# Performance work log

Measured on AMD Instinct MI355X. Metric: run time of the kernel, lower is better.

## Reference

```python
import jax, jax.numpy as jnp
import numpy as np

N, E, D, H, O = 50000, 800000, 128, 128, 64


def setup_inputs() -> dict:
    key = jax.random.key(0)
    ks = jax.random.split(key, 16)
    x = jax.random.normal(ks[0], (N, D), jnp.float32)
    edge_index = jax.random.randint(ks[1], (2, E), 0, N, dtype=jnp.int32).astype(jnp.int64)

    def lin_w(k, out_d, in_d):
        return jax.random.normal(k, (out_d, in_d), jnp.float32) * (1.0 / np.sqrt(in_d))

    return {
        "x": x,
        "edge_index": edge_index,
        # SAGEConv layer 0 (D -> H): lin_l acts on aggregated neighbors (with bias), lin_r on root (no bias)
        "Wl0": lin_w(ks[2], H, D), "bl0": jnp.zeros((H,), jnp.float32), "Wr0": lin_w(ks[3], H, D),
        # SAGEConv layers 1,2 (H -> H)
        "Wl1": lin_w(ks[4], H, H), "bl1": jnp.zeros((H,), jnp.float32), "Wr1": lin_w(ks[5], H, H),
        "Wl2": lin_w(ks[6], H, H), "bl2": jnp.zeros((H,), jnp.float32), "Wr2": lin_w(ks[7], H, H),
        # post_mp: Linear(H,H) -> Dropout -> Linear(H,O)
        "Wp1": lin_w(ks[8], H, H), "bp1": jnp.zeros((H,), jnp.float32),
        "Wp2": lin_w(ks[9], O, H), "bp2": jnp.zeros((O,), jnp.float32),
    }


def _sage_conv(x, src, dst, W_l, b_l, W_r, n_nodes):
    # mean-aggregate neighbor features: scatter messages x[src] onto dst
    msgs = x[src]                                              # [E, F] gather
    agg = jax.ops.segment_sum(msgs, dst, num_segments=n_nodes)  # [N, F]
    cnt = jax.ops.segment_sum(jnp.ones((src.shape[0],), x.dtype), dst, num_segments=n_nodes)
    mean = agg / jnp.maximum(cnt, 1.0)[:, None]
    return mean @ W_l.T + b_l + x @ W_r.T


def reference(x, edge_index, Wl0, bl0, Wr0, Wl1, bl1, Wr1, Wl2, bl2, Wr2, Wp1, bp1, Wp2, bp2):
    src, dst = edge_index[0], edge_index[1]
    n_nodes = x.shape[0]
    layers = [(Wl0, bl0, Wr0), (Wl1, bl1, Wr1), (Wl2, bl2, Wr2)]
    h = x
    for (W_l, b_l, W_r) in layers:
        h = _sage_conv(h, src, dst, W_l, b_l, W_r, n_nodes)
        h = jax.nn.relu(h)
        # dropout is identity at inference (training=False)
    h = h @ Wp1.T + bp1
    h = h @ Wp2.T + bp2
    return jax.nn.log_softmax(h, axis=1)
```

## Files before the change

kernel.cpp:

```cpp
#include <hip/hip_runtime.h>

using s16x8 = __attribute__((ext_vector_type(8))) short;
using f32x4 = __attribute__((ext_vector_type(4))) float;

#define NBUKMAX 512
#define BCAP    3072
#define CHUNK   4096

static __device__ __forceinline__ float bf2f(unsigned short u){
  union { unsigned int i; float f; } v; v.i = ((unsigned)u) << 16; return v.f;
}
static __device__ __forceinline__ unsigned short f2bf(float f){
  union { float f; unsigned int i; } v; v.f = f;
  unsigned int x = v.i;
  return (unsigned short)((x + 0x7fffu + ((x >> 16) & 1u)) >> 16);
}

__global__ __launch_bounds__(256) void k_bscatter(const int* __restrict__ ei, int E,
                                                  int* __restrict__ gcur,
                                                  unsigned int* __restrict__ tmp){
  __shared__ unsigned int pk[CHUNK];
  __shared__ unsigned short bk[CHUNK];
  __shared__ int hist[NBUKMAX];
  __shared__ int cur[NBUKMAX];
  __shared__ int sh64;
  int tid = threadIdx.x;
  if (tid == 0) sh64 = 1;
  for (int j = tid; j < NBUKMAX; j += 256) hist[j] = 0;
  __syncthreads();
  {
    int nc = E < 64 ? E : 64;
    if (tid < nc && ei[2*tid + 1] != 0) sh64 = 0;
  }
  __syncthreads();
  int is64 = sh64;
  int base = blockIdx.x * CHUNK;
  int m = E - base; if (m > CHUNK) m = CHUNK;
  for (int j = tid; j < m; j += 256){
    int i = base + j;
    int s = is64 ? ei[2*(size_t)i] : ei[i];
    int d = is64 ? ei[2*((size_t)E + i)] : ei[(size_t)E + i];
    pk[j] = ((unsigned)(d & 127) << 25) | (unsigned)s;
    int b = d >> 7;
    bk[j] = (unsigned short)b;
    atomicAdd(&hist[b], 1);
  }
  __syncthreads();
  for (int b = tid; b < NBUKMAX; b += 256){
    int r = hist[b];
    cur[b] = (r > 0) ? atomicAdd(&gcur[b], r) : 0;
  }
  __syncthreads();
  for (int j = tid; j < m; j += 256){
    int b = bk[j];
    int p = atomicAdd(&cur[b], 1);
    if (p < BCAP) tmp[(size_t)b*BCAP + p] = pk[j];
  }
}

__global__ __launch_bounds__(256) void k_binfill(const unsigned int* __restrict__ tmp,
                                                 const int* __restrict__ gcur,
                                                 int* __restrict__ rowp,
                                                 int* __restrict__ srcs, int N, int nbk){
  __shared__ int hist[128], cur[128];
  __shared__ unsigned int stg[BCAP];
  __shared__ int lout[BCAP];
  __shared__ int sh_obase;
  int b = blockIdx.x;
  int d0 = b << 7;
  int nd = N - d0; if (nd > 128) nd = 128;
  int n = gcur[b]; if (n > BCAP) n = BCAP; if (n < 0) n = 0;
  int tid = threadIdx.x;
  for (int j = tid; j < 128; j += 256) hist[j] = 0;
  if (tid < 64){
    int lane = tid;
    int carry = 0;
    for (int b0 = 0; b0 <= b; b0 += 64){
      int bb = b0 + lane;
      int sz = 0;
      if (bb < nbk){ sz = gcur[bb]; if (sz > BCAP) sz = BCAP; if (sz < 0) sz = 0; }
      int s = sz;
      #pragma unroll
      for (int off = 1; off < 64; off <<= 1){
        int u = __shfl_up(s, off, 64);
        if (lane >= off) s += u;
      }
      if (bb == b) sh_obase = carry + s - sz;
      carry += __shfl(s, 63, 64);
    }
  }
  __syncthreads();
  int obase = sh_obase;
  const unsigned int* reg = tmp + (size_t)b * BCAP;
  for (int i = tid; i < n; i += 256){
    unsigned int w = reg[i];
    stg[i] = w;
    atomicAdd(&hist[w >> 25], 1);
  }
  __syncthreads();
  if (tid < 64){
    int a  = hist[2*tid];
    int b2 = hist[2*tid+1];
    int ps = a + b2;
    int s = ps;
    #pragma unroll
    for (int off = 1; off < 64; off <<= 1){
      int u = __shfl_up(s, off, 64);
      if (tid >= off) s += u;
    }
    int ep = s - ps;
    cur[2*tid]   = ep;
    cur[2*tid+1] = ep + a;
    if (2*tid   < nd) rowp[d0 + 2*tid]   = obase + ep;
    if (2*tid+1 < nd) rowp[d0 + 2*tid+1] = obase + ep + a;
  }
  if (b == nbk - 1 && tid == 0) rowp[N] = obase + n;
  __syncthreads();
  for (int i = tid; i < n; i += 256){
    unsigned int w = stg[i];
    int p = atomicAdd(&cur[w >> 25], 1);
    lout[p] = (int)(w & 0x1FFFFFFu);
  }
  __syncthreads();
  for (int i = tid; i < n; i += 256) srcs[obase + i] = lout[i];
}

__global__ __launch_bounds__(256) void k_prep(const float* __restrict__ x, unsigned short* __restrict__ xb, int n4, int nx,
                                              const float* __restrict__ w0, const float* __restrict__ w1,
                                              const float* __restrict__ w2, const float* __restrict__ w3,
                                              const float* __restrict__ w4, const float* __restrict__ w5,
                                              unsigned short* __restrict__ o0, unsigned short* __restrict__ o1,
                                              unsigned short* __restrict__ o2, unsigned short* __restrict__ o3,
                                              unsigned short* __restrict__ o4, unsigned short* __restrict__ o5,
                                              const float* __restrict__ Wp1, const float* __restrict__ bp1,
                                              const float* __restrict__ Wp2, const float* __restrict__ bp2,
                                              unsigned short* __restrict__ Wc, float* __restrict__ bc){
  int bx = blockIdx.x;
  if (bx < nx){
    int i = bx*256 + threadIdx.x;
    if (i >= n4) return;
    float4 v = ((const float4*)x)[i];
    ushort4 o; o.x = f2bf(v.x); o.y = f2bf(v.y); o.z = f2bf(v.z); o.w = f2bf(v.w);
    ((ushort4*)xb)[i] = o;
  } else if (bx < nx + 96){
    int w = bx - nx;
    int job = w >> 4, blk = w & 15;
    const float* in; unsigned short* out;
    switch (job){
      case 0: in = w0; out = o0; break;
      case 1: in = w1; out = o1; break;
      case 2: in = w2; out = o2; break;
      case 3: in = w3; out = o3; break;
      case 4: in = w4; out = o4; break;
      default: in = w5; out = o5; break;
    }
    int i = blk*256 + threadIdx.x;
    float4 v = ((const float4*)in)[i];
    ushort4 o; o.x = f2bf(v.x); o.y = f2bf(v.y); o.z = f2bf(v.z); o.w = f2bf(v.w);
    ((ushort4*)out)[i] = o;
  } else {
    int idx = (bx - nx - 96)*256 + threadIdx.x;
    if (idx >= 64*128) return;
    int o = idx >> 7, k = idx & 127;
    float s = 0.f;
    for (int j = 0; j < 128; ++j) s += Wp2[o*128 + j] * Wp1[j*128 + k];
    Wc[o*128 + k] = f2bf(s);
    if (k == 0){
      float t = bp2[o];
      for (int j = 0; j < 128; ++j) t += Wp2[o*128 + j] * bp1[j];
      bc[o] = t;
    }
  }
}

__global__ __launch_bounds__(256) void k_agg(const unsigned short* __restrict__ h,
                                             const int* __restrict__ rowp,
                                             const int* __restrict__ srcs,
                                             unsigned short* __restrict__ mean, int N){
  int wv = blockIdx.x*4 + (threadIdx.x >> 6);
  int n0 = wv*2;
  if (n0 >= N) return;
  int n1 = n0 + 1;
  int lane = threadIdx.x & 63;
  int g  = lane >> 4;
  int fl = lane & 15;
  int beg0 = rowp[n0], end0 = rowp[n0+1];
  int beg1 = beg0, end1 = beg0;
  if (n1 < N){ beg1 = rowp[n1]; end1 = rowp[n1+1]; }
  int deg0 = end0 - beg0, deg1 = end1 - beg1;
  int it0 = (deg0 + 15) >> 4, it1 = (deg1 + 15) >> 4;
  int it = it0 > it1 ? it0 : it1;
  int c0 = deg0 > 0 ? end0 - 1 : 0;
  int c1 = deg1 > 0 ? end1 - 1 : 0;
  float a0[8], a1[8];
  #pragma unroll
  for (int f = 0; f < 8; ++f){ a0[f] = 0.f; a1[f] = 0.f; }
  for (int t = 0; t < it; ++t){
    int b0 = beg0 + t*16, b1 = beg1 + t*16;
    int si0[4], si1[4]; float w0[4], w1[4];
    #pragma unroll
    for (int s = 0; s < 4; ++s){
      int sl0 = b0 + s*4 + g;
      w0[s] = (sl0 < end0) ? 1.f : 0.f;
      si0[s] = srcs[sl0 < end0 ? sl0 : c0];
      int sl1 = b1 + s*4 + g;
      w1[s] = (sl1 < end1) ? 1.f : 0.f;
      si1[s] = srcs[sl1 < end1 ? sl1 : c1];
    }
    uint4 v0[4], v1[4];
    #pragma unroll
    for (int s = 0; s < 4; ++s) v0[s] = *(const uint4*)(h + (size_t)si0[s]*128 + fl*8);
    #pragma unroll
    for (int s = 0; s < 4; ++s) v1[s] = *(const uint4*)(h + (size_t)si1[s]*128 + fl*8);
    #pragma unroll
    for (int s = 0; s < 4; ++s){
      #pragma unroll
      for (int q = 0; q < 4; ++q){
        unsigned int wd = ((const unsigned int*)&v0[s])[q];
        a0[2*q]   = fmaf(w0[s], bf2f((unsigned short)(wd & 0xffffu)), a0[2*q]);
        a0[2*q+1] = fmaf(w0[s], bf2f((unsigned short)(wd >> 16)),     a0[2*q+1]);
        wd = ((const unsigned int*)&v1[s])[q];
        a1[2*q]   = fmaf(w1[s], bf2f((unsigned short)(wd & 0xffffu)), a1[2*q]);
        a1[2*q+1] = fmaf(w1[s], bf2f((unsigned short)(wd >> 16)),     a1[2*q+1]);
      }
    }
  }
  #pragma unroll
  for (int f = 0; f < 8; ++f){
    a0[f] += __shfl_xor(a0[f], 16, 64);
    a0[f] += __shfl_xor(a0[f], 32, 64);
    a1[f] += __shfl_xor(a1[f], 16, 64);
    a1[f] += __shfl_xor(a1[f], 32, 64);
  }
  if (g == 0){
    float inv0 = deg0 > 0 ? 1.f/(float)deg0 : 0.f;
    unsigned int o[4];
    #pragma unroll
    for (int q = 0; q < 4; ++q)
      o[q] = ((unsigned int)f2bf(a0[2*q+1]*inv0) << 16) | f2bf(a0[2*q]*inv0);
    *(uint4*)(mean + (size_t)n0*128 + fl*8) = *(uint4*)&o[0];
    if (n1 < N){
      float inv1 = deg1 > 0 ? 1.f/(float)deg1 : 0.f;
      #pragma unroll
      for (int q = 0; q < 4; ++q)
        o[q] = ((unsigned int)f2bf(a1[2*q+1]*inv1) << 16) | f2bf(a1[2*q]*inv1);
      *(uint4*)(mean + (size_t)n1*128 + fl*8) = *(uint4*)&o[0];
    }
  }
}

__global__ __launch_bounds__(256) void k_gemm(const unsigned short* __restrict__ mean,
                                              const unsigned short* __restrict__ hin,
                                              const unsigned short* __restrict__ Wl,
                                              const unsigned short* __restrict__ Wr,
                                              const float* __restrict__ bias,
                                              unsigned short* __restrict__ hout, int N){
  __shared__ unsigned short wlds[64*512];
  int wave = threadIdx.x >> 6;
  int lane = threadIdx.x & 63;
  int lr = lane & 15;
  int kg = lane >> 4;

  #pragma unroll
  for (int cc = 0; cc < 16; ++cc){
    int c = wave + cc*4;
    const unsigned short* W = (c < 32) ? Wl : Wr;
    int jt = (c >> 2) & 7, t = c & 3;
    s16x8 v = *(const s16x8*)(W + (size_t)(jt*16 + lr)*128 + t*32 + kg*8);
    *(s16x8*)(wlds + (size_t)c*512 + lane*8) = v;
  }
  __syncthreads();

  int row0 = (blockIdx.x*4 + wave) * 16;
  if (row0 >= N) return;
  int row = row0 + lr; if (row >= N) row = N - 1;

  s16x8 a[8];
  const unsigned short* mrow = mean + (size_t)row*128;
  const unsigned short* hrow = hin  + (size_t)row*128;
  #pragma unroll
  for (int t = 0; t < 4; ++t) a[t]   = *(const s16x8*)(mrow + t*32 + kg*8);
  #pragma unroll
  for (int t = 0; t < 4; ++t) a[4+t] = *(const s16x8*)(hrow + t*32 + kg*8);

  #pragma unroll
  for (int jt = 0; jt < 8; ++jt){
    f32x4 acc = {0.f, 0.f, 0.f, 0.f};
    #pragma unroll
    for (int t = 0; t < 4; ++t){
      s16x8 b = *(const s16x8*)(wlds + (size_t)(jt*4 + t)*512 + lane*8);
      acc = __builtin_amdgcn_mfma_f32_16x16x32_bf16(a[t], b, acc, 0, 0, 0);
    }
    #pragma unroll
    for (int t = 0; t < 4; ++t){
      s16x8 b = *(const s16x8*)(wlds + (size_t)(32 + jt*4 + t)*512 + lane*8);
      acc = __builtin_amdgcn_mfma_f32_16x16x32_bf16(a[4+t], b, acc, 0, 0, 0);
    }
    int ocol = jt*16 + lr;
    float bv = bias[ocol];
    #pragma unroll
    for (int i = 0; i < 4; ++i){
      int orow = row0 + kg*4 + i;
      if (orow < N){
        float v = acc[i] + bv;
        v = fmaxf(v, 0.f);
        hout[(size_t)orow*128 + ocol] = f2bf(v);
      }
    }
  }
}

__global__ __launch_bounds__(256) void k_gemmpost(const unsigned short* __restrict__ mean,
                                                  const unsigned short* __restrict__ hin,
                                                  const unsigned short* __restrict__ Wl,
                                                  const unsigned short* __restrict__ Wr,
                                                  const float* __restrict__ bias,
                                                  const unsigned short* __restrict__ Wc,
                                                  const float* __restrict__ bc,
                                                  float* __restrict__ out, int N){
  __shared__ unsigned short wlds[64*512];
  int wave = threadIdx.x >> 6;
  int lane = threadIdx.x & 63;
  int lr = lane & 15;
  int kg = lane >> 4;

  #pragma unroll
  for (int cc = 0; cc < 16; ++cc){
    int c = wave + cc*4;
    const unsigned short* W = (c < 32) ? Wl : Wr;
    int jt = (c >> 2) & 7, t = c & 3;
    s16x8 v = *(const s16x8*)(W + (size_t)(jt*16 + lr)*128 + t*32 + kg*8);
    *(s16x8*)(wlds + (size_t)c*512 + lane*8) = v;
  }
  __syncthreads();

  int row0 = (blockIdx.x*4 + wave) * 16;
  int row = row0 + lr; if (row >= N) row = N - 1;

  s16x8 a[8];
  const unsigned short* mrow = mean + (size_t)row*128;
  const unsigned short* hrow = hin  + (size_t)row*128;
  #pragma unroll
  for (int t = 0; t < 4; ++t) a[t]   = *(const s16x8*)(mrow + t*32 + kg*8);
  #pragma unroll
  for (int t = 0; t < 4; ++t) a[4+t] = *(const s16x8*)(hrow + t*32 + kg*8);

  f32x4 acc2[8];
  #pragma unroll
  for (int jt = 0; jt < 8; ++jt){
    f32x4 acc = {0.f, 0.f, 0.f, 0.f};
    #pragma unroll
    for (int t = 0; t < 4; ++t){
      s16x8 b = *(const s16x8*)(wlds + (size_t)(jt*4 + t)*512 + lane*8);
      acc = __builtin_amdgcn_mfma_f32_16x16x32_bf16(a[t], b, acc, 0, 0, 0);
    }
    #pragma unroll
    for (int t = 0; t < 4; ++t){
      s16x8 b = *(const s16x8*)(wlds + (size_t)(32 + jt*4 + t)*512 + lane*8);
      acc = __builtin_amdgcn_mfma_f32_16x16x32_bf16(a[4+t], b, acc, 0, 0, 0);
    }
    acc2[jt] = acc;
  }
  __syncthreads();

  unsigned short* tl = wlds + (size_t)wave * (16*136);
  #pragma unroll
  for (int jt = 0; jt < 8; ++jt){
    float bv = bias[jt*16 + lr];
    #pragma unroll
    for (int i = 0; i < 4; ++i){
      float v = fmaxf(acc2[jt][i] + bv, 0.f);
      tl[(kg*4 + i)*136 + jt*16 + lr] = f2bf(v);
    }
  }
  s16x8 am[4];
  #pragma unroll
  for (int t = 0; t < 4; ++t)
    am[t] = *(const s16x8*)(tl + lr*136 + t*32 + kg*8);

  float vv[4][4];
  #pragma unroll
  for (int jt = 0; jt < 4; ++jt){
    f32x4 acc = {0.f, 0.f, 0.f, 0.f};
    const unsigned short* wrow = Wc + (size_t)(jt*16 + lr)*128;
    #pragma unroll
    for (int t = 0; t < 4; ++t){
      s16x8 b = *(const s16x8*)(wrow + t*32 + kg*8);
      acc = __builtin_amdgcn_mfma_f32_16x16x32_bf16(am[t], b, acc, 0, 0, 0);
    }
    float bv = bc[jt*16 + lr];
    #pragma unroll
    for (int i = 0; i < 4; ++i) vv[jt][i] = acc[i] + bv;
  }

  #pragma unroll
  for (int i = 0; i < 4; ++i){
    float m = vv[0][i];
    #pragma unroll
    for (int jt = 1; jt < 4; ++jt) m = fmaxf(m, vv[jt][i]);
    #pragma unroll
    for (int msk = 1; msk < 16; msk <<= 1) m = fmaxf(m, __shfl_xor(m, msk, 64));
    float s = 0.f;
    #pragma unroll
    for (int jt = 0; jt < 4; ++jt) s += expf(vv[jt][i] - m);
    #pragma unroll
    for (int msk = 1; msk < 16; msk <<= 1) s += __shfl_xor(s, msk, 64);
    float lse = m + logf(s);
    int orow = row0 + kg*4 + i;
    if (orow < N){
      #pragma unroll
      for (int jt = 0; jt < 4; ++jt)
        out[(size_t)orow*64 + jt*16 + lr] = vv[jt][i] - lse;
    }
  }
}

extern "C" void kernel_launch(void* const* d_in, const int* in_sizes, int n_in,
                              void* d_out, int out_size, void* d_ws, size_t ws_size,
                              hipStream_t stream){
  const int N = in_sizes[0] / 128;
  const int E = in_sizes[1] / 2;
  if (N <= 0 || E <= 0) return;

  const float* x   = (const float*)d_in[0];
  const int*   ei  = (const int*)d_in[1];
  const float* Wl[3] = {(const float*)d_in[2], (const float*)d_in[5], (const float*)d_in[8]};
  const float* bl[3] = {(const float*)d_in[3], (const float*)d_in[6], (const float*)d_in[9]};
  const float* Wr[3] = {(const float*)d_in[4], (const float*)d_in[7], (const float*)d_in[10]};
  const float* Wp1 = (const float*)d_in[11];
  const float* bp1 = (const float*)d_in[12];
  const float* Wp2 = (const float*)d_in[13];
  const float* bp2 = (const float*)d_in[14];
  float* out = (float*)d_out;

  char* p = (char*)d_ws;
  auto alloc = [&](size_t bytes){ char* r = p; p += (bytes + 255) & ~(size_t)255; return r; };
  unsigned short* xb   = (unsigned short*)alloc((size_t)N*128*2);
  unsigned short* hA   = (unsigned short*)alloc((size_t)N*128*2);
  unsigned short* hB   = (unsigned short*)alloc((size_t)N*128*2);
  unsigned short* mean = (unsigned short*)alloc((size_t)N*128*2);
  unsigned short* wlb[3], *wrb[3];
  for (int l = 0; l < 3; ++l){
    wlb[l] = (unsigned short*)alloc(128*128*2);
    wrb[l] = (unsigned short*)alloc(128*128*2);
  }
  unsigned short* wc = (unsigned short*)alloc(64*128*2);
  float* bc   = (float*)alloc(64*4);
  int* rowp   = (int*)alloc((size_t)(N+1)*4);
  int* srcs   = (int*)alloc((size_t)E*4);
  int* gcur   = (int*)alloc((size_t)NBUKMAX*4);
  unsigned int* tmp = (unsigned int*)alloc((size_t)NBUKMAX*BCAP*4);

  int nbk = (N + 127) >> 7;

  hipMemsetAsync(gcur, 0, (size_t)NBUKMAX*4, stream);
  k_bscatter<<<(E + CHUNK - 1)/CHUNK, 256, 0, stream>>>(ei, E, gcur, tmp);
  k_binfill<<<nbk, 256, 0, stream>>>(tmp, gcur, rowp, srcs, N, nbk);

  int n4 = N*128/4;
  int nx = (n4 + 255)/256;
  k_prep<<<nx + 96 + 32, 256, 0, stream>>>(x, xb, n4, nx,
                                           Wl[0], Wr[0], Wl[1], Wr[1], Wl[2], Wr[2],
                                           wlb[0], wrb[0], wlb[1], wrb[1], wlb[2], wrb[2],
                                           Wp1, bp1, Wp2, bp2, wc, bc);

  int waves = (N + 15)/16;
  int gblocks = (waves + 3)/4;
  int ablocks = (N + 7)/8;
  k_agg<<<ablocks, 256, 0, stream>>>(xb, rowp, srcs, mean, N);
  k_gemm<<<gblocks, 256, 0, stream>>>(mean, xb, wlb[0], wrb[0], bl[0], hA, N);
  k_agg<<<ablocks, 256, 0, stream>>>(hA, rowp, srcs, mean, N);
  k_gemm<<<gblocks, 256, 0, stream>>>(mean, hA, wlb[1], wrb[1], bl[1], hB, N);
  k_agg<<<ablocks, 256, 0, stream>>>(hB, rowp, srcs, mean, N);
  k_gemmpost<<<gblocks, 256, 0, stream>>>(mean, hB, wlb[2], wrb[2], bl[2], wc, bc, out, N);
}
```

Baseline: 212.3 us.

## Merge edge bucketing with prep kernel and aggregate one node per wave

The edge-bucket scatter kernel and the bf16 conversion/weight-prep kernel become one launch, so the independent front-end work shares a grid and one launch is dropped. The aggregation kernel now gives each wave a single node instead of two interleaved nodes, with an early exit for zero-degree nodes, and doubles the aggregation grid. This removes the wasted iterations spent padding the shorter of two neighbour lists. In exchange there is less memory-level parallelism per wave, and the fused front kernel reserves the scatter path's shared memory for every block.

```diff
diff --git a/kernel.cpp b/kernel.cpp
--- a/kernel.cpp
+++ b/kernel.cpp
@@ -16,45 +16,92 @@
   return (unsigned short)((x + 0x7fffu + ((x >> 16) & 1u)) >> 16);
 }
 
-__global__ __launch_bounds__(256) void k_bscatter(const int* __restrict__ ei, int E,
-                                                  int* __restrict__ gcur,
-                                                  unsigned int* __restrict__ tmp){
-  __shared__ unsigned int pk[CHUNK];
-  __shared__ unsigned short bk[CHUNK];
-  __shared__ int hist[NBUKMAX];
-  __shared__ int cur[NBUKMAX];
-  __shared__ int sh64;
+__global__ __launch_bounds__(256) void k_front(const int* __restrict__ ei, int E, int nbs,
+                                               int* __restrict__ gcur, unsigned int* __restrict__ tmp,
+                                               const float* __restrict__ x, unsigned short* __restrict__ xb,
+                                               int n4, int nx,
+                                               const float* __restrict__ w0, const float* __restrict__ w1,
+                                               const float* __restrict__ w2, const float* __restrict__ w3,
+                                               const float* __restrict__ w4, const float* __restrict__ w5,
+                                               unsigned short* __restrict__ o0, unsigned short* __restrict__ o1,
+                                               unsigned short* __restrict__ o2, unsigned short* __restrict__ o3,
+                                               unsigned short* __restrict__ o4, unsigned short* __restrict__ o5,
+                                               const float* __restrict__ Wp1, const float* __restrict__ bp1,
+                                               const float* __restrict__ Wp2, const float* __restrict__ bp2,
+                                               unsigned short* __restrict__ Wc, float* __restrict__ bc){
+  int bx = blockIdx.x;
   int tid = threadIdx.x;
-  if (tid == 0) sh64 = 1;
-  for (int j = tid; j < NBUKMAX; j += 256) hist[j] = 0;
-  __syncthreads();
-  {
-    int nc = E < 64 ? E : 64;
-    if (tid < nc && ei[2*tid + 1] != 0) sh64 = 0;
-  }
-  __syncthreads();
-  int is64 = sh64;
-  int base = blockIdx.x * CHUNK;
-  int m = E - base; if (m > CHUNK) m = CHUNK;
-  for (int j = tid; j < m; j += 256){
-    int i = base + j;
-    int s = is64 ? ei[2*(size_t)i] : ei[i];
-    int d = is64 ? ei[2*((size_t)E + i)] : ei[(size_t)E + i];
-    pk[j] = ((unsigned)(d & 127) << 25) | (unsigned)s;
-    int b = d >> 7;
-    bk[j] = (unsigned short)b;
-    atomicAdd(&hist[b], 1);
-  }
-  __syncthreads();
-  for (int b = tid; b < NBUKMAX; b += 256){
-    int r = hist[b];
-    cur[b] = (r > 0) ? atomicAdd(&gcur[b], r) : 0;
-  }
-  __syncthreads();
-  for (int j = tid; j < m; j += 256){
-    int b = bk[j];
-    int p = atomicAdd(&cur[b], 1);
-    if (p < BCAP) tmp[(size_t)b*BCAP + p] = pk[j];
+  if (bx < nbs){
+    __shared__ unsigned int pk[CHUNK];
+    __shared__ unsigned short bk[CHUNK];
+    __shared__ int hist[NBUKMAX];
+    __shared__ int cur[NBUKMAX];
+    __shared__ int sh64;
+    if (tid == 0) sh64 = 1;
+    for (int j = tid; j < NBUKMAX; j += 256) hist[j] = 0;
+    __syncthreads();
+    {
+      int nc = E < 64 ? E : 64;
+      if (tid < nc && ei[2*tid + 1] != 0) sh64 = 0;
+    }
+    __syncthreads();
+    int is64 = sh64;
+    int base = bx * CHUNK;
+    int m = E - base; if (m > CHUNK) m = CHUNK;
+    for (int j = tid; j < m; j += 256){
+      int i = base + j;
+      int s = is64 ? ei[2*(size_t)i] : ei[i];
+      int d = is64 ? ei[2*((size_t)E + i)] : ei[(size_t)E + i];
+      pk[j] = ((unsigned)(d & 127) << 25) | (unsigned)s;
+      int b = d >> 7;
+      bk[j] = (unsigned short)b;
+      atomicAdd(&hist[b], 1);
+    }
+    __syncthreads();
+    for (int b = tid; b < NBUKMAX; b += 256){
+      int r = hist[b];
+      cur[b] = (r > 0) ? atomicAdd(&gcur[b], r) : 0;
+    }
+    __syncthreads();
+    for (int j = tid; j < m; j += 256){
+      int b = bk[j];
+      int p = atomicAdd(&cur[b], 1);
+      if (p < BCAP) tmp[(size_t)b*BCAP + p] = pk[j];
+    }
+  } else if (bx < nbs + nx){
+    int i = (bx - nbs)*256 + tid;
+    if (i >= n4) return;
+    float4 v = ((const float4*)x)[i];
+    ushort4 o; o.x = f2bf(v.x); o.y = f2bf(v.y); o.z = f2bf(v.z); o.w = f2bf(v.w);
+    ((ushort4*)xb)[i] = o;
+  } else if (bx < nbs + nx + 96){
+    int w = bx - nbs - nx;
+    int job = w >> 4, blk = w & 15;
+    const float* in; unsigned short* out;
+    switch (job){
+      case 0: in = w0; out = o0; break;
+      case 1: in = w1; out = o1; break;
+      case 2: in = w2; out = o2; break;
+      case 3: in = w3; out = o3; break;
+      case 4: in = w4; out = o4; break;
+      default: in = w5; out = o5; break;
+    }
+    int i = blk*256 + tid;
+    float4 v = ((const float4*)in)[i];
+    ushort4 o; o.x = f2bf(v.x); o.y = f2bf(v.y); o.z = f2bf(v.z); o.w = f2bf(v.w);
+    ((ushort4*)out)[i] = o;
+  } else {
+    int idx = (bx - nbs - nx - 96)*256 + tid;
+    if (idx >= 64*128) return;
+    int o = idx >> 7, k = idx & 127;
+    float s = 0.f;
+    for (int j = 0; j < 128; ++j) s += Wp2[o*128 + j] * Wp1[j*128 + k];
+    Wc[o*128 + k] = f2bf(s);
+    if (k == 0){
+      float t = bp2[o];
+      for (int j = 0; j < 128; ++j) t += Wp2[o*128 + j] * bp1[j];
+      bc[o] = t;
+    }
   }
 }
 
@@ -125,127 +172,60 @@
   for (int i = tid; i < n; i += 256) srcs[obase + i] = lout[i];
 }
 
-__global__ __launch_bounds__(256) void k_prep(const float* __restrict__ x, unsigned short* __restrict__ xb, int n4, int nx,
-                                              const float* __restrict__ w0, const float* __restrict__ w1,
-                                              const float* __restrict__ w2, const float* __restrict__ w3,
-                                              const float* __restrict__ w4, const float* __restrict__ w5,
-                                              unsigned short* __restrict__ o0, unsigned short* __restrict__ o1,
-                                              unsigned short* __restrict__ o2, unsigned short* __restrict__ o3,
-                                              unsigned short* __restrict__ o4, unsigned short* __restrict__ o5,
-                                              const float* __restrict__ Wp1, const float* __restrict__ bp1,
-                                              const float* __restrict__ Wp2, const float* __restrict__ bp2,
-                                              unsigned short* __restrict__ Wc, float* __restrict__ bc){
-  int bx = blockIdx.x;
-  if (bx < nx){
-    int i = bx*256 + threadIdx.x;
-    if (i >= n4) return;
-    float4 v = ((const float4*)x)[i];
-    ushort4 o; o.x = f2bf(v.x); o.y = f2bf(v.y); o.z = f2bf(v.z); o.w = f2bf(v.w);
-    ((ushort4*)xb)[i] = o;
-  } else if (bx < nx + 96){
-    int w = bx - nx;
-    int job = w >> 4, blk = w & 15;
-    const float* in; unsigned short* out;
-    switch (job){
-      case 0: in = w0; out = o0; break;
-      case 1: in = w1; out = o1; break;
-      case 2: in = w2; out = o2; break;
-      case 3: in = w3; out = o3; break;
-      case 4: in = w4; out = o4; break;
-      default: in = w5; out = o5; break;
-    }
-    int i = blk*256 + threadIdx.x;
-    float4 v = ((const float4*)in)[i];
-    ushort4 o; o.x = f2bf(v.x); o.y = f2bf(v.y); o.z = f2bf(v.z); o.w = f2bf(v.w);
-    ((ushort4*)out)[i] = o;
-  } else {
-    int idx = (bx - nx - 96)*256 + threadIdx.x;
-    if (idx >= 64*128) return;
-    int o = idx >> 7, k = idx & 127;
-    float s = 0.f;
-    for (int j = 0; j < 128; ++j) s += Wp2[o*128 + j] * Wp1[j*128 + k];
-    Wc[o*128 + k] = f2bf(s);
-    if (k == 0){
-      float t = bp2[o];
-      for (int j = 0; j < 128; ++j) t += Wp2[o*128 + j] * bp1[j];
-      bc[o] = t;
-    }
-  }
-}
-
 __global__ __launch_bounds__(256) void k_agg(const unsigned short* __restrict__ h,
                                              const int* __restrict__ rowp,
                                              const int* __restrict__ srcs,
                                              unsigned short* __restrict__ mean, int N){
-  int wv = blockIdx.x*4 + (threadIdx.x >> 6);
-  int n0 = wv*2;
-  if (n0 >= N) return;
-  int n1 = n0 + 1;
+  int node = blockIdx.x*4 + (threadIdx.x >> 6);
+  if (node >= N) return;
   int lane = threadIdx.x & 63;
   int g  = lane >> 4;
   int fl = lane & 15;
-  int beg0 = rowp[n0], end0 = rowp[n0+1];
-  int beg1 = beg0, end1 = beg0;
-  if (n1 < N){ beg1 = rowp[n1]; end1 = rowp[n1+1]; }
-  int deg0 = end0 - beg0, deg1 = end1 - beg1;
-  int it0 = (deg0 + 15) >> 4, it1 = (deg1 + 15) >> 4;
-  int it = it0 > it1 ? it0 : it1;
-  int c0 = deg0 > 0 ? end0 - 1 : 0;
-  int c1 = deg1 > 0 ? end1 - 1 : 0;
-  float a0[8], a1[8];
-  #pragma unroll
-  for (int f = 0; f < 8; ++f){ a0[f] = 0.f; a1[f] = 0.f; }
-  for (int t = 0; t < it; ++t){
-    int b0 = beg0 + t*16, b1 = beg1 + t*16;
-    int si0[4], si1[4]; float w0[4], w1[4];
+  int beg = rowp[node], end = rowp[node+1];
+  int deg = end - beg;
+  if (deg <= 0){
+    if (g == 0){
+      uint4 z = make_uint4(0,0,0,0);
+      *(uint4*)(mean + (size_t)node*128 + fl*8) = z;
+    }
+    return;
+  }
+  float acc[8];
+  #pragma unroll
+  for (int f = 0; f < 8; ++f) acc[f] = 0.f;
+  int last = end - 1;
+  for (int base = beg; base < end; base += 16){
+    int si[4]; float w[4]; uint4 v[4];
     #pragma unroll
     for (int s = 0; s < 4; ++s){
-      int sl0 = b0 + s*4 + g;
-      w0[s] = (sl0 < end0) ? 1.f : 0.f;
-      si0[s] = srcs[sl0 < end0 ? sl0 : c0];
-      int sl1 = b1 + s*4 + g;
-      w1[s] = (sl1 < end1) ? 1.f : 0.f;
-      si1[s] = srcs[sl1 < end1 ? sl1 : c1];
-    }
-    uint4 v0[4], v1[4];
-    #pragma unroll
-    for (int s = 0; s < 4; ++s) v0[s] = *(const uint4*)(h + (size_t)si0[s]*128 + fl*8);
-    #pragma unroll
-    for (int s = 0; s < 4; ++s) v1[s] = *(const uint4*)(h + (size_t)si1[s]*128 + fl*8);
+      int sl = base + s*4 + g;
+      w[s] = (sl < end) ? 1.f : 0.f;
+      si[s] = srcs[sl < end ? sl : last];
+    }
+    #pragma unroll
+    for (int s = 0; s < 4; ++s) v[s] = *(const uint4*)(h + (size_t)si[s]*128 + fl*8);
     #pragma unroll
     for (int s = 0; s < 4; ++s){
       #pragma unroll
       for (int q = 0; q < 4; ++q){
-        unsigned int wd = ((const unsigned int*)&v0[s])[q];
-        a0[2*q]   = fmaf(w0[s], bf2f((unsigned short)(wd & 0xffffu)), a0[2*q]);
-        a0[2*q+1] = fmaf(w0[s], bf2f((unsigned short)(wd >> 16)),     a0[2*q+1]);
-        wd = ((const unsigned int*)&v1[s])[q];
-        a1[2*q]   = fmaf(w1[s], bf2f((unsigned short)(wd & 0xffffu)), a1[2*q]);
-        a1[2*q+1] = fmaf(w1[s], bf2f((unsigned short)(wd >> 16)),     a1[2*q+1]);
+        unsigned int wd = ((const unsigned int*)&v[s])[q];
+        acc[2*q]   = fmaf(w[s], bf2f((unsigned short)(wd & 0xffffu)), acc[2*q]);
+        acc[2*q+1] = fmaf(w[s], bf2f((unsigned short)(wd >> 16)),     acc[2*q+1]);
       }
     }
   }
   #pragma unroll
   for (int f = 0; f < 8; ++f){
-    a0[f] += __shfl_xor(a0[f], 16, 64);
-    a0[f] += __shfl_xor(a0[f], 32, 64);
-    a1[f] += __shfl_xor(a1[f], 16, 64);
-    a1[f] += __shfl_xor(a1[f], 32, 64);
+    acc[f] += __shfl_xor(acc[f], 16, 64);
+    acc[f] += __shfl_xor(acc[f], 32, 64);
   }
   if (g == 0){
-    float inv0 = deg0 > 0 ? 1.f/(float)deg0 : 0.f;
+    float inv = 1.f / (float)deg;
     unsigned int o[4];
     #pragma unroll
     for (int q = 0; q < 4; ++q)
-      o[q] = ((unsigned int)f2bf(a0[2*q+1]*inv0) << 16) | f2bf(a0[2*q]*inv0);
-    *(uint4*)(mean + (size_t)n0*128 + fl*8) = *(uint4*)&o[0];
-    if (n1 < N){
-      float inv1 = deg1 > 0 ? 1.f/(float)deg1 : 0.f;
-      #pragma unroll
-      for (int q = 0; q < 4; ++q)
-        o[q] = ((unsigned int)f2bf(a1[2*q+1]*inv1) << 16) | f2bf(a1[2*q]*inv1);
-      *(uint4*)(mean + (size_t)n1*128 + fl*8) = *(uint4*)&o[0];
-    }
+      o[q] = ((unsigned int)f2bf(acc[2*q+1]*inv) << 16) | f2bf(acc[2*q]*inv);
+    *(uint4*)(mean + (size_t)node*128 + fl*8) = *(uint4*)&o[0];
   }
 }
 
@@ -452,21 +432,21 @@
   unsigned int* tmp = (unsigned int*)alloc((size_t)NBUKMAX*BCAP*4);
 
   int nbk = (N + 127) >> 7;
-
-  hipMemsetAsync(gcur, 0, (size_t)NBUKMAX*4, stream);
-  k_bscatter<<<(E + CHUNK - 1)/CHUNK, 256, 0, stream>>>(ei, E, gcur, tmp);
-  k_binfill<<<nbk, 256, 0, stream>>>(tmp, gcur, rowp, srcs, N, nbk);
-
+  int nbs = (E + CHUNK - 1)/CHUNK;
   int n4 = N*128/4;
   int nx = (n4 + 255)/256;
-  k_prep<<<nx + 96 + 32, 256, 0, stream>>>(x, xb, n4, nx,
-                                           Wl[0], Wr[0], Wl[1], Wr[1], Wl[2], Wr[2],
-                                           wlb[0], wrb[0], wlb[1], wrb[1], wlb[2], wrb[2],
-                                           Wp1, bp1, Wp2, bp2, wc, bc);
+
+  hipMemsetAsync(gcur, 0, (size_t)NBUKMAX*4, stream);
+  k_front<<<nbs + nx + 96 + 32, 256, 0, stream>>>(ei, E, nbs, gcur, tmp,
+                                                  x, xb, n4, nx,
+                                                  Wl[0], Wr[0], Wl[1], Wr[1], Wl[2], Wr[2],
+                                                  wlb[0], wrb[0], wlb[1], wrb[1], wlb[2], wrb[2],
+                                                  Wp1, bp1, Wp2, bp2, wc, bc);
+  k_binfill<<<nbk, 256, 0, stream>>>(tmp, gcur, rowp, srcs, N, nbk);
 
   int waves = (N + 15)/16;
   int gblocks = (waves + 3)/4;
-  int ablocks = (N + 7)/8;
+  int ablocks = (N + 3)/4;
   k_agg<<<ablocks, 256, 0, stream>>>(xb, rowp, srcs, mean, N);
   k_gemm<<<gblocks, 256, 0, stream>>>(mean, xb, wlb[0], wrb[0], bl[0], hA, N);
   k_agg<<<ablocks, 256, 0, stream>>>(hA, rowp, srcs, mean, N);
```

Result: faster. 189.4 us, median of 2 (-10.8%).
